# Kernel optimization log

Hardware: AMD Instinct MI355X
Metric: run time of the kernel (lower is better)

## Reference

```python
import jax, jax.numpy as jnp
import numpy as np

B, N, D, H, C = 1, 256, 128, 4, 32
EPS = 1e-5

def setup_inputs() -> dict:
    key = jax.random.key(0)
    ks = jax.random.split(key, 10)
    s = 1.0 / np.sqrt(D)
    return {
        "Z_raw": jax.random.normal(ks[0], (B, N, N, D), dtype=jnp.float32),
        "Z_mask": jnp.ones((B, N, N), dtype=jnp.float32),
        "ln_w": jnp.ones((D,), dtype=jnp.float32),
        "ln_b": jnp.zeros((D,), dtype=jnp.float32),
        "b_proj_w": (jax.random.normal(ks[1], (H, D), dtype=jnp.float32) * s),
        "wq": jax.random.normal(ks[2], (D, H * C), dtype=jnp.float32) * s,
        "wk": jax.random.normal(ks[3], (D, H * C), dtype=jnp.float32) * s,
        "wv": jax.random.normal(ks[4], (D, H * C), dtype=jnp.float32) * s,
        "wg": jax.random.normal(ks[5], (D, H * C), dtype=jnp.float32) * s,
        "bg": jnp.ones((H * C,), dtype=jnp.float32),  # FastFold inits gating bias to 1
        "wo": jax.random.normal(ks[6], (H * C, D), dtype=jnp.float32) / np.sqrt(H * C),
        "out_bias": jnp.zeros((D,), dtype=jnp.float32),
    }

def reference(Z_raw, Z_mask, ln_w, ln_b, b_proj_w, wq, wk, wv, wg, bg, wo, out_bias):
    # LayerNorm over d_pair
    mu = jnp.mean(Z_raw, axis=-1, keepdims=True)
    var = jnp.mean(jnp.square(Z_raw - mu), axis=-1, keepdims=True)
    Z = (Z_raw - mu) * jax.lax.rsqrt(var + EPS) * ln_w + ln_b  # [B,N,N,D]

    # Triangle bias: b[b,h,q,k] (shared across rows i)
    tb = jnp.einsum('bqkd,hd->bhqk', Z, b_proj_w)  # [B,H,N,N]

    scale = 1.0 / np.sqrt(C)
    q = jnp.einsum('bijd,de->bije', Z, wq).reshape(B, N, N, H, C) * scale
    k = jnp.einsum('bijd,de->bije', Z, wk).reshape(B, N, N, H, C)
    v = jnp.einsum('bijd,de->bije', Z, wv).reshape(B, N, N, H, C)

    logits = jnp.einsum('biqhc,bikhc->bihqk', q, k)  # [B,I,H,N,N]
    mask_bias = 1e9 * (Z_mask - 1.0)  # [B,I,J]
    logits = logits + mask_bias[:, :, None, None, :] + tb[:, None]
    attn = jax.nn.softmax(logits, axis=-1)

    o = jnp.einsum('bihqk,bikhc->biqhc', attn, v)  # [B,I,N,H,C]
    gate = jax.nn.sigmoid(jnp.einsum('bijd,de->bije', Z, wg) + bg)
    o = o.reshape(B, N, N, H * C) * gate
    out = jnp.einsum('bije,ed->bijd', o, wo)

    # bias_dropout_add (eval mode: dropout is identity; dropout_mask is ones)
    return Z_raw + out + out_bias
```

## Files before the change

### kernel.cpp

```cpp
#include <hip/hip_runtime.h>
#include <hip/hip_bf16.h>


#define NN 256
#define DD 128
#define NP (NN*NN)

typedef __hip_bfloat16 bf16;
typedef unsigned short u16;
typedef unsigned int u32;
typedef __bf16 bf16x8 __attribute__((ext_vector_type(8)));
typedef short s16x4 __attribute__((ext_vector_type(4)));
typedef float f32x4 __attribute__((ext_vector_type(4)));

__device__ __forceinline__ float b2f(bf16 x) { return __bfloat162float(x); }
__device__ __forceinline__ bf16 f2b(float x) { return __float2bfloat16(x); }
__device__ __forceinline__ float lo16(u32 u) { return __uint_as_float(u << 16); }
__device__ __forceinline__ float hi16(u32 u) { return __uint_as_float(u & 0xFFFF0000u); }
__device__ __forceinline__ float fexp2(float x) { return __builtin_amdgcn_exp2f(x); }
__device__ __forceinline__ bool bf16_mode(const void* lnw_raw) {
    return ((const u32*)lnw_raw)[0] == 0x3F803F80u;
}
__device__ __forceinline__ u32 pk2(float a, float b) {
    union { bf16 h; u16 u; } ca, cb; ca.h = f2b(a); cb.h = f2b(b);
    return ((u32)cb.u << 16) | (u32)ca.u;
}
__device__ __forceinline__ bf16x8 ld_frag(const u32* p) {
    uint4 r = *(const uint4*)p;
    return __builtin_bit_cast(bf16x8, r);
}
#define MFMA16(a,b,c) __builtin_amdgcn_mfma_f32_16x16x32_bf16(a,b,c,0,0,0)
#define MFMA16K(a,b,c) __builtin_amdgcn_mfma_f32_16x16x16bf16_1k(a,b,c,0,0,0)
#define PLANE(et) (((size_t)(et)) << 19)

#define OFF_ZM    0
#define OFF_LNW   65536
#define OFF_LNB   65664
#define OFF_BPW   65792
#define OFF_WQ    66304
#define OFF_WK    82688
#define OFF_WV    99072
#define OFF_WG    115456
#define OFF_BG    131840
#define OFF_WO    131968
#define OFF_OBIAS 148352
#define CANON_TOTAL 148480
#define OFF_WQT   148480
#define OFF_WKT   164864
#define OFF_WVT   181248
#define OFF_WGT   197632
#define OFF_WOT   214016
#define CANONT_TOTAL 81920

#define SCALE 0.17677669529663687f
#define LOG2E 1.4426950408889634f

__global__ __launch_bounds__(256) void k_conv(
    const void* zm, const void* lnw, const void* lnb, const void* bpw,
    const void* wq, const void* wk, const void* wv, const void* wg,
    const void* bg, const void* wo, const void* obias, bf16* canon)
{
    const bool bfm = bf16_mode(lnw);
    int idx = blockIdx.x * 256 + threadIdx.x;
    if (idx < CANON_TOTAL) {
        const void* src; int off;
        if      (idx < OFF_LNW)   { src = zm;    off = idx; }
        else if (idx < OFF_LNB)   { src = lnw;   off = idx - OFF_LNW; }
        else if (idx < OFF_BPW)   { src = lnb;   off = idx - OFF_LNB; }
        else if (idx < OFF_WQ)    { src = bpw;   off = idx - OFF_BPW; }
        else if (idx < OFF_WK)    { src = wq;    off = idx - OFF_WQ; }
        else if (idx < OFF_WV)    { src = wk;    off = idx - OFF_WK; }
        else if (idx < OFF_WG)    { src = wv;    off = idx - OFF_WV; }
        else if (idx < OFF_BG)    { src = wg;    off = idx - OFF_WG; }
        else if (idx < OFF_WO)    { src = bg;    off = idx - OFF_BG; }
        else if (idx < OFF_OBIAS) { src = wo;    off = idx - OFF_WO; }
        else                      { src = obias; off = idx - OFF_OBIAS; }
        float f = bfm ? b2f(((const bf16*)src)[off]) : ((const float*)src)[off];
        if (idx >= OFF_BPW && idx < OFF_WQ) f *= LOG2E;
        if (idx >= OFF_BG  && idx < OFF_WO) f *= LOG2E;
        canon[idx] = f2b(f);
    } else if (idx < CANON_TOTAL + CANONT_TOTAL) {
        int i2 = idx - CANON_TOTAL;
        int m = i2 >> 14, r = i2 & 16383;
        int a = r >> 7, b = r & 127;
        const void* s = (m==0) ? wq : (m==1) ? wk : (m==2) ? wv
                      : (m==3) ? wg : wo;
        float v = bfm ? b2f(((const bf16*)s)[b*128 + a])
                      : ((const float*)s)[b*128 + a];
        if (m == 0) v *= SCALE*LOG2E;
        if (m == 3) v *= LOG2E;
        canon[OFF_WQT + i2] = f2b(v);
    }
}

__global__ __launch_bounds__(256, 4) void k_ln_qkv(
    const void* __restrict__ Zr, const void* __restrict__ lnw_raw,
    const bf16* __restrict__ canon,
    u32* __restrict__ qbw, u32* __restrict__ kbw,
    u32* __restrict__ vbTw, u32* __restrict__ gbw, bf16* __restrict__ tbw)
{
    __shared__ u32 zs[64*68];
    const bool bfm = bf16_mode(lnw_raw);
    const u32* cw = (const u32*)canon;
    const int t = threadIdx.x;
    const int base = blockIdx.x * 64;
    const int p = t >> 2, l = t & 3;
    const int pair = base + p;

    float vals[32];
    if (bfm) {
        const u32* zr = (const u32*)Zr + (size_t)pair*64 + l*16;
        #pragma unroll
        for (int j = 0; j < 16; ++j) {
            u32 u = zr[j];
            vals[2*j] = lo16(u); vals[2*j+1] = hi16(u);
        }
    } else {
        const float* zr = (const float*)Zr + (size_t)pair*128 + l*32;
        #pragma unroll
        for (int j = 0; j < 32; ++j) vals[j] = zr[j];
    }

    float s = 0.f;
    #pragma unroll
    for (int m = 0; m < 32; ++m) s += vals[m];
    s += __shfl_xor(s, 1); s += __shfl_xor(s, 2);
    const float mu = s * (1.f/128.f);
    float s2 = 0.f;
    #pragma unroll
    for (int m = 0; m < 32; ++m) { float d = vals[m] - mu; s2 += d*d; }
    s2 += __shfl_xor(s2, 1); s2 += __shfl_xor(s2, 2);
    const float rstd = rsqrtf(s2 * (1.f/128.f) + 1e-5f);

    const u32* lnw_w = cw + (OFF_LNW>>1) + l*16;
    const u32* lnb_w = cw + (OFF_LNB>>1) + l*16;
    #pragma unroll
    for (int j = 0; j < 16; ++j) {
        u32 uw = lnw_w[j], ub = lnb_w[j];
        float z0 = (vals[2*j]  -mu)*rstd*lo16(uw) + lo16(ub);
        float z1 = (vals[2*j+1]-mu)*rstd*hi16(uw) + hi16(ub);
        zs[p*68 + l*16 + j] = pk2(z0, z1);
    }
    __syncthreads();

    const int wv_ = t >> 6, lane = t & 63, qn = lane & 15, quad = lane >> 4;

    {
        f32x4 dtb = {0.f,0.f,0.f,0.f};
        #pragma unroll
        for (int ks = 0; ks < 4; ++ks) {
            bf16x8 a = ld_frag(cw + (OFF_BPW>>1) + qn*64 + ks*16 + quad*4);
            bf16x8 zbq = ld_frag(&zs[(wv_*16+qn)*68 + ks*16 + quad*4]);
            dtb = MFMA16(a, zbq, dtb);
        }
        if (quad == 0) {
            const int pc = base + wv_*16 + qn;
            tbw[0*NP + pc] = f2b(dtb[0]);
            tbw[1*NP + pc] = f2b(dtb[1]);
            tbw[2*NP + pc] = f2b(dtb[2]);
            tbw[3*NP + pc] = f2b(dtb[3]);
        }
    }

    const int ib = base >> 8;
    const int jbase = (base & 255);

    #pragma unroll
    for (int ei = 0; ei < 2; ++ei) {
        const int et = wv_*2 + ei;
        bf16x8 aq[4], ak[4], av[4], ag[4];
        #pragma unroll
        for (int ks = 0; ks < 4; ++ks) {
            aq[ks] = ld_frag(cw + (OFF_WQT>>1) + (et*16+qn)*64 + ks*16 + quad*4);
            ak[ks] = ld_frag(cw + (OFF_WKT>>1) + (et*16+qn)*64 + ks*16 + quad*4);
            av[ks] = ld_frag(cw + (OFF_WVT>>1) + (et*16+qn)*64 + ks*16 + quad*4);
            ag[ks] = ld_frag(cw + (OFF_WGT>>1) + (et*16+qn)*64 + ks*16 + quad*4);
        }
        const uint2 bgv = *(const uint2*)(cw + (OFF_BG>>1) + et*8 + quad*2);
        const int e = et*16 + qn;
        u32* vrow = vbTw + (size_t)((ib*4 + (e>>5))*32 + (e&31))*128;
        #pragma unroll
        for (int pg = 0; pg < 4; ++pg) {
            bf16x8 zb[4];
            #pragma unroll
            for (int ks = 0; ks < 4; ++ks)
                zb[ks] = ld_frag(&zs[(pg*16+qn)*68 + ks*16 + quad*4]);
            f32x4 dq = {0.f,0.f,0.f,0.f}, dk = {0.f,0.f,0.f,0.f};
            f32x4 dv = {0.f,0.f,0.f,0.f}, dg = {0.f,0.f,0.f,0.f};
            #pragma unroll
            for (int ks = 0; ks < 4; ++ks) {
                dq = MFMA16(aq[ks], zb[ks], dq);
                dk = MFMA16(ak[ks], zb[ks], dk);
                dv = MFMA16(zb[ks], av[ks], dv);
                dg = MFMA16(ag[ks], zb[ks], dg);
            }
            const size_t pr = (size_t)(base + pg*16 + qn)*8 + quad*2;
            uint2 sq; sq.x = pk2(dq[0], dq[1]); sq.y = pk2(dq[2], dq[3]);
            *(uint2*)(qbw + PLANE(et) + pr) = sq;
            uint2 sk; sk.x = pk2(dk[0], dk[1]); sk.y = pk2(dk[2], dk[3]);
            *(uint2*)(kbw + PLANE(et) + pr) = sk;
            float g0 = 1.f / (1.f + fexp2(-(dg[0] + lo16(bgv.x))));
            float g1 = 1.f / (1.f + fexp2(-(dg[1] + hi16(bgv.x))));
            float g2 = 1.f / (1.f + fexp2(-(dg[2] + lo16(bgv.y))));
            float g3 = 1.f / (1.f + fexp2(-(dg[3] + hi16(bgv.y))));
            uint2 sg; sg.x = pk2(g0, g1); sg.y = pk2(g2, g3);
            *(uint2*)(gbw + PLANE(et) + pr) = sg;
            const int jj = jbase + pg*16 + quad*4;
            uint2 sv2; sv2.x = pk2(dv[0], dv[1]); sv2.y = pk2(dv[2], dv[3]);
            *(uint2*)(vrow + (jj>>1)) = sv2;
        }
    }
}

__global__ __launch_bounds__(256, 4) void k_attn(
    const u32* __restrict__ qb, u32* __restrict__ kb,
    const u32* __restrict__ vbT, const bf16* __restrict__ canon,
    const bf16* __restrict__ tbw, const u32* __restrict__ gb)
{
    __shared__ u32 ks_s[256*16];
    __shared__ u32 vs_s[32*128];
    __shared__ float mb_s[256];
    const int t = threadIdx.x;
    const int i = blockIdx.x & 255, h = blockIdx.x >> 8;

    {
        const uint4* kp0 = (const uint4*)(kb + PLANE(2*h)   + (size_t)i*2048);
        const uint4* kp1 = (const uint4*)(kb + PLANE(2*h+1) + (size_t)i*2048);
        #pragma unroll
        for (int r = 0; r < 2; ++r) {
            int q4 = t + 256*r;
            int p = q4 >> 1;
            int c0 = (q4 & 1);
            int c1 = 2 + (q4 & 1);
            uint4 a = kp0[q4];
            *(uint4*)&ks_s[p*16 + ((c0 + (p>>1)) & 3)*4] = a;
            uint4 b = kp1[q4];
            *(uint4*)&ks_s[p*16 + ((c1 + (p>>1)) & 3)*4] = b;
        }
    }
    #pragma unroll
    for (int r = 0; r < 4; ++r) {
        int u = t + 256*r;
        int row = u >> 5, d4 = (u & 31)*4;
        *(uint4*)&vs_s[row*128 + (d4 ^ ((row & 7) << 2))] =
            *(const uint4*)(vbT + (size_t)((i*4+h)*32 + row)*128 + d4);
    }
    {
        u32 w = ((const u32*)canon)[(OFF_ZM>>1) + i*128 + (t>>1)];
        float m = (t & 1) ? hi16(w) : lo16(w);
        mb_s[t] = 1.4426950e9f * (m - 1.f);
    }
    __syncthreads();

    const int wave = t >> 6, lane = t & 63;
    const int qn = lane & 15, quad = lane >> 4;
    const int ksw = ((quad + (qn>>1)) & 3) * 4;
    const int vswz = (qn & 7) << 2;

    const u32* tbbase = (const u32*)tbw + ((size_t)h*NP >> 1) + (wave*64+qn)*128 + quad*2;

    uint2 tA[8], tB[8];
    #pragma unroll
    for (int kk = 0; kk < 8; ++kk) tA[kk] = *(const uint2*)(tbbase + kk*8);

    #pragma unroll
    for (int qt = 0; qt < 4; ++qt) {
        const int qg = wave*64 + qt*16 + qn;
        bf16x8 qf = ld_frag(qb + PLANE(2*h + (quad>>1)) + (size_t)(i*256+qg)*8 + (quad&1)*4);

        float sum = 0.f;
        f32x4 o0a = {0.f,0.f,0.f,0.f}, o0b = {0.f,0.f,0.f,0.f};
        f32x4 o1a = {0.f,0.f,0.f,0.f}, o1b = {0.f,0.f,0.f,0.f};

        {
            f32x4 sv8[8];
            #pragma unroll
            for (int kk = 0; kk < 8; ++kk) {
                f32x4 mb4 = *(const f32x4*)&mb_s[kk*16 + quad*4];
                sv8[kk][0] = lo16(tA[kk].x) + mb4[0];
                sv8[kk][1] = hi16(tA[kk].x) + mb4[1];
                sv8[kk][2] = lo16(tA[kk].y) + mb4[2];
                sv8[kk][3] = hi16(tA[kk].y) + mb4[3];
            }
            #pragma unroll
            for (int kk = 0; kk < 8; ++kk)
                tB[kk] = *(const uint2*)(tbbase + qt*2048 + (8+kk)*8);
            #pragma unroll
            for (int kk = 0; kk < 8; ++kk) {
                bf16x8 kf = ld_frag(&ks_s[(kk*16+qn)*16 + ksw]);
                sv8[kk] = MFMA16(kf, qf, sv8[kk]);
            }
            #pragma unroll
            for (int kk = 0; kk < 8; ++kk) {
                float e0 = fexp2(sv8[kk][0]);
                float e1 = fexp2(sv8[kk][1]);
                float e2 = fexp2(sv8[kk][2]);
                float e3 = fexp2(sv8[kk][3]);
                sum += (e0 + e1) + (e2 + e3);
                uint2 pw2; pw2.x = pk2(e0, e1); pw2.y = pk2(e2, e3);
                s16x4 pf = __builtin_bit_cast(s16x4, pw2);
                const int vcol = (kk*8 + quad*2) ^ vswz;
                s16x4 v0 = __builtin_bit_cast(s16x4, *(const uint2*)&vs_s[qn*128 + vcol]);
                s16x4 v1 = __builtin_bit_cast(s16x4, *(const uint2*)&vs_s[(16+qn)*128 + vcol]);
                if (kk & 1) {
                    o0b = MFMA16K(v0, pf, o0b);
                    o1b = MFMA16K(v1, pf, o1b);
                } else {
                    o0a = MFMA16K(v0, pf, o0a);
                    o1a = MFMA16K(v1, pf, o1a);
                }
            }
            __builtin_amdgcn_sched_barrier(0);
        }
        {
            f32x4 sv8[8];
            #pragma unroll
            for (int kk = 0; kk < 8; ++kk) {
                f32x4 mb4 = *(const f32x4*)&mb_s[(8+kk)*16 + quad*4];
                sv8[kk][0] = lo16(tB[kk].x) + mb4[0];
                sv8[kk][1] = hi16(tB[kk].x) + mb4[1];
                sv8[kk][2] = lo16(tB[kk].y) + mb4[2];
                sv8[kk][3] = hi16(tB[kk].y) + mb4[3];
            }
            if (qt < 3) {
                #pragma unroll
                for (int kk = 0; kk < 8; ++kk)
                    tA[kk] = *(const uint2*)(tbbase + (qt+1)*2048 + kk*8);
            }
            #pragma unroll
            for (int kk = 0; kk < 8; ++kk) {
                const int kt = 8 + kk;
                bf16x8 kf = ld_frag(&ks_s[(kt*16+qn)*16 + ksw]);
                sv8[kk] = MFMA16(kf, qf, sv8[kk]);
            }
            #pragma unroll
            for (int kk = 0; kk < 8; ++kk) {
                const int kt = 8 + kk;
                float e0 = fexp2(sv8[kk][0]);
                float e1 = fexp2(sv8[kk][1]);
                float e2 = fexp2(sv8[kk][2]);
                float e3 = fexp2(sv8[kk][3]);
                sum += (e0 + e1) + (e2 + e3);
                uint2 pw2; pw2.x = pk2(e0, e1); pw2.y = pk2(e2, e3);
                s16x4 pf = __builtin_bit_cast(s16x4, pw2);
                const int vcol = (kt*8 + quad*2) ^ vswz;
                s16x4 v0 = __builtin_bit_cast(s16x4, *(const uint2*)&vs_s[qn*128 + vcol]);
                s16x4 v1 = __builtin_bit_cast(s16x4, *(const uint2*)&vs_s[(16+qn)*128 + vcol]);
                if (kk & 1) {
                    o0b = MFMA16K(v0, pf, o0b);
                    o1b = MFMA16K(v1, pf, o1b);
                } else {
                    o0a = MFMA16K(v0, pf, o0a);
                    o1a = MFMA16K(v1, pf, o1a);
                }
            }
            __builtin_amdgcn_sched_barrier(0);
        }
        sum += __shfl_xor(sum, 16);
        sum += __shfl_xor(sum, 32);
        f32x4 o0 = o0a + o0b;
        f32x4 o1 = o1a + o1b;

        const u32* gpb = gb + PLANE(2*h) + (size_t)(i*256+qg)*8 + quad*2;
        uint2 ga = *(const uint2*)gpb;
        uint2 gc = *(const uint2*)(gpb + (1u<<19));
        const float rinv = 1.f / sum;
        uint2 s0, s1;
        s0.x = pk2(o0[0]*rinv*lo16(ga.x), o0[1]*rinv*hi16(ga.x));
        s0.y = pk2(o0[2]*rinv*lo16(ga.y), o0[3]*rinv*hi16(ga.y));
        s1.x = pk2(o1[0]*rinv*lo16(gc.x), o1[1]*rinv*hi16(gc.x));
        s1.y = pk2(o1[2]*rinv*lo16(gc.y), o1[3]*rinv*hi16(gc.y));
        u32* opb = kb + PLANE(2*h) + (size_t)(i*256+qg)*8 + quad*2;
        *(uint2*)opb = s0;
        *(uint2*)(opb + (1u<<19)) = s1;
    }
}

__global__ __launch_bounds__(256, 4) void k_out(
    const void* __restrict__ Zr, const void* __restrict__ lnw_raw,
    const bf16* __restrict__ canon,
    const u32* __restrict__ obg, void* __restrict__ outp)
{
    const bool bfm = bf16_mode(lnw_raw);
    const u32* cw = (const u32*)canon;
    const int t = threadIdx.x;
    const int base = blockIdx.x * 64;
    const int wv_ = t >> 6, lane = t & 63, qn = lane & 15, quad = lane >> 4;

    bf16x8 awo[2][4];
    uint2 oi2[2];
    #pragma unroll
    for (int di = 0; di < 2; ++di) {
        const int dt = wv_*2 + di;
        #pragma unroll
        for (int ks = 0; ks < 4; ++ks)
            awo[di][ks] = ld_frag(cw + (OFF_WOT>>1) + (dt*16+qn)*64 + ks*16 + quad*4);
        oi2[di] = *(const uint2*)(cw + (OFF_OBIAS>>1) + dt*8 + quad*2);
    }
    #pragma unroll
    for (int pg = 0; pg < 4; ++pg) {
        const size_t pair = base + pg*16 + qn;
        const size_t prow = pair*64;
        bf16x8 ogb[4];
        #pragma unroll
        for (int ks = 0; ks < 4; ++ks)
            ogb[ks] = ld_frag(obg + PLANE(2*ks + (quad>>1)) + pair*8 + (quad&1)*4);
        #pragma unroll
        for (int di = 0; di < 2; ++di) {
            const int dt = wv_*2 + di;
            f32x4 ao = {0.f,0.f,0.f,0.f};
            #pragma unroll
            for (int ks = 0; ks < 4; ++ks) ao = MFMA16(awo[di][ks], ogb[ks], ao);
            const float b0 = lo16(oi2[di].x), b1 = hi16(oi2[di].x);
            const float b2v = lo16(oi2[di].y), b3 = hi16(oi2[di].y);
            if (bfm) {
                uint2 zr2 = *(const uint2*)((const u32*)Zr + prow + dt*8 + quad*2);
                uint2 w;
                w.x = pk2(ao[0] + b0 + lo16(zr2.x), ao[1] + b1 + hi16(zr2.x));
                w.y = pk2(ao[2] + b2v + lo16(zr2.y), ao[3] + b3 + hi16(zr2.y));
                *(uint2*)((u32*)outp + prow + dt*8 + quad*2) = w;
            } else {
                const float* zr = (const float*)Zr + pair*128 + dt*16 + quad*4;
                float4 z4 = *(const float4*)zr;
                float4 w;
                w.x = ao[0] + b0 + z4.x;  w.y = ao[1] + b1 + z4.y;
                w.z = ao[2] + b2v + z4.z; w.w = ao[3] + b3 + z4.w;
                *(float4*)((float*)outp + pair*128 + dt*16 + quad*4) = w;
            }
        }
    }
}

extern "C" void kernel_launch(void* const* d_in, const int* in_sizes, int n_in,
                              void* d_out, int out_size, void* d_ws, size_t ws_size,
                              hipStream_t stream)
{
    const void* Zr    = d_in[0];
    const void* Zm    = d_in[1];
    const void* lnw   = d_in[2];
    const void* lnb   = d_in[3];
    const void* bpw   = d_in[4];
    const void* wq    = d_in[5];
    const void* wk    = d_in[6];
    const void* wv    = d_in[7];
    const void* wg    = d_in[8];
    const void* bg    = d_in[9];
    const void* wo    = d_in[10];
    const void* obias = d_in[11];

    char* ws = (char*)d_ws;
    const size_t M = 16777216;
    u32* gbw   = (u32*)(ws);
    u32* qbw   = (u32*)(ws + 1*M);
    u32* kbw   = (u32*)(ws + 2*M);
    u32* vbTw  = (u32*)(ws + 3*M);
    bf16* tbw  = (bf16*)(ws + 5*M);
    bf16* canon = (bf16*)(ws + 5*M + 1048576);

    hipLaunchKernelGGL(k_conv, dim3((CANON_TOTAL+CANONT_TOTAL+255)/256), dim3(256),
                       0, stream,
                       Zm, lnw, lnb, bpw, wq, wk, wv, wg, bg, wo, obias, canon);
    hipLaunchKernelGGL(k_ln_qkv, dim3(1024), dim3(256), 0, stream,
                       Zr, lnw, canon, qbw, kbw, vbTw, gbw, tbw);
    hipLaunchKernelGGL(k_attn, dim3(1024), dim3(256), 0, stream,
                       qbw, kbw, vbTw, canon, tbw, gbw);
    hipLaunchKernelGGL(k_out, dim3(1024), dim3(256), 0, stream,
                       Zr, lnw, canon, kbw, d_out);
}
```

Baseline: 179.1 us.

## Split attention blocks over query halves and read mask directly from global

The attention grid is doubled so each block handles two of the four query tiles per (row, head), with launch bounds raised to allow more resident blocks. Two blocks now read the same K plane, so the output is written to a separate workspace buffer instead of overwriting K, and the output kernel reads from that buffer. The mask-bias LDS staging is removed; mask values are loaded from global memory and folded in with an fma. The aim is more parallelism and occupancy to hide latency. The cost is that every block still stages the full K and V into LDS, so that traffic doubles.

```diff
diff --git a/kernel.cpp b/kernel.cpp
--- a/kernel.cpp
+++ b/kernel.cpp
@@ -32,6 +32,7 @@
 #define MFMA16(a,b,c) __builtin_amdgcn_mfma_f32_16x16x32_bf16(a,b,c,0,0,0)
 #define MFMA16K(a,b,c) __builtin_amdgcn_mfma_f32_16x16x16bf16_1k(a,b,c,0,0,0)
 #define PLANE(et) (((size_t)(et)) << 19)
+#define BIGC 1.4426950e9f
 
 #define OFF_ZM    0
 #define OFF_LNW   65536
@@ -212,16 +213,17 @@
     }
 }
 
-__global__ __launch_bounds__(256, 4) void k_attn(
-    const u32* __restrict__ qb, u32* __restrict__ kb,
+__global__ __launch_bounds__(256, 5) void k_attn(
+    const u32* __restrict__ qb, const u32* __restrict__ kb,
     const u32* __restrict__ vbT, const bf16* __restrict__ canon,
-    const bf16* __restrict__ tbw, const u32* __restrict__ gb)
+    const bf16* __restrict__ tbw, const u32* __restrict__ gb,
+    u32* __restrict__ ob)
 {
     __shared__ u32 ks_s[256*16];
     __shared__ u32 vs_s[32*128];
-    __shared__ float mb_s[256];
     const int t = threadIdx.x;
-    const int i = blockIdx.x & 255, h = blockIdx.x >> 8;
+    const int i = blockIdx.x & 255, h = (blockIdx.x >> 8) & 3;
+    const int qh = blockIdx.x >> 10;
 
     {
         const uint4* kp0 = (const uint4*)(kb + PLANE(2*h)   + (size_t)i*2048);
@@ -245,11 +247,6 @@
         *(uint4*)&vs_s[row*128 + (d4 ^ ((row & 7) << 2))] =
             *(const uint4*)(vbT + (size_t)((i*4+h)*32 + row)*128 + d4);
     }
-    {
-        u32 w = ((const u32*)canon)[(OFF_ZM>>1) + i*128 + (t>>1)];
-        float m = (t & 1) ? hi16(w) : lo16(w);
-        mb_s[t] = 1.4426950e9f * (m - 1.f);
-    }
     __syncthreads();
 
     const int wave = t >> 6, lane = t & 63;
@@ -257,14 +254,17 @@
     const int ksw = ((quad + (qn>>1)) & 3) * 4;
     const int vswz = (qn & 7) << 2;
 
+    const u32* zmr = (const u32*)canon + (OFF_ZM>>1) + i*128 + quad*2;
     const u32* tbbase = (const u32*)tbw + ((size_t)h*NP >> 1) + (wave*64+qn)*128 + quad*2;
 
     uint2 tA[8], tB[8];
     #pragma unroll
-    for (int kk = 0; kk < 8; ++kk) tA[kk] = *(const uint2*)(tbbase + kk*8);
-
-    #pragma unroll
-    for (int qt = 0; qt < 4; ++qt) {
+    for (int kk = 0; kk < 8; ++kk)
+        tA[kk] = *(const uint2*)(tbbase + qh*2*2048 + kk*8);
+
+    #pragma unroll
+    for (int qi = 0; qi < 2; ++qi) {
+        const int qt = qh*2 + qi;
         const int qg = wave*64 + qt*16 + qn;
         bf16x8 qf = ld_frag(qb + PLANE(2*h + (quad>>1)) + (size_t)(i*256+qg)*8 + (quad&1)*4);
 
@@ -276,11 +276,11 @@
             f32x4 sv8[8];
             #pragma unroll
             for (int kk = 0; kk < 8; ++kk) {
-                f32x4 mb4 = *(const f32x4*)&mb_s[kk*16 + quad*4];
-                sv8[kk][0] = lo16(tA[kk].x) + mb4[0];
-                sv8[kk][1] = hi16(tA[kk].x) + mb4[1];
-                sv8[kk][2] = lo16(tA[kk].y) + mb4[2];
-                sv8[kk][3] = hi16(tA[kk].y) + mb4[3];
+                uint2 zm2 = *(const uint2*)(zmr + kk*8);
+                sv8[kk][0] = fmaf(BIGC, lo16(zm2.x) - 1.f, lo16(tA[kk].x));
+                sv8[kk][1] = fmaf(BIGC, hi16(zm2.x) - 1.f, hi16(tA[kk].x));
+                sv8[kk][2] = fmaf(BIGC, lo16(zm2.y) - 1.f, lo16(tA[kk].y));
+                sv8[kk][3] = fmaf(BIGC, hi16(zm2.y) - 1.f, hi16(tA[kk].y));
             }
             #pragma unroll
             for (int kk = 0; kk < 8; ++kk)
@@ -316,13 +316,14 @@
             f32x4 sv8[8];
             #pragma unroll
             for (int kk = 0; kk < 8; ++kk) {
-                f32x4 mb4 = *(const f32x4*)&mb_s[(8+kk)*16 + quad*4];
-                sv8[kk][0] = lo16(tB[kk].x) + mb4[0];
-                sv8[kk][1] = hi16(tB[kk].x) + mb4[1];
-                sv8[kk][2] = lo16(tB[kk].y) + mb4[2];
-                sv8[kk][3] = hi16(tB[kk].y) + mb4[3];
-            }
-            if (qt < 3) {
+                const int kt = 8 + kk;
+                uint2 zm2 = *(const uint2*)(zmr + kt*8);
+                sv8[kk][0] = fmaf(BIGC, lo16(zm2.x) - 1.f, lo16(tB[kk].x));
+                sv8[kk][1] = fmaf(BIGC, hi16(zm2.x) - 1.f, hi16(tB[kk].x));
+                sv8[kk][2] = fmaf(BIGC, lo16(zm2.y) - 1.f, lo16(tB[kk].y));
+                sv8[kk][3] = fmaf(BIGC, hi16(zm2.y) - 1.f, hi16(tB[kk].y));
+            }
+            if (qi < 1) {
                 #pragma unroll
                 for (int kk = 0; kk < 8; ++kk)
                     tA[kk] = *(const uint2*)(tbbase + (qt+1)*2048 + kk*8);
@@ -370,7 +371,7 @@
         s0.y = pk2(o0[2]*rinv*lo16(ga.y), o0[3]*rinv*hi16(ga.y));
         s1.x = pk2(o1[0]*rinv*lo16(gc.x), o1[1]*rinv*hi16(gc.x));
         s1.y = pk2(o1[2]*rinv*lo16(gc.y), o1[3]*rinv*hi16(gc.y));
-        u32* opb = kb + PLANE(2*h) + (size_t)(i*256+qg)*8 + quad*2;
+        u32* opb = ob + PLANE(2*h) + (size_t)(i*256+qg)*8 + quad*2;
         *(uint2*)opb = s0;
         *(uint2*)(opb + (1u<<19)) = s1;
     }
@@ -454,6 +455,7 @@
     u32* qbw   = (u32*)(ws + 1*M);
     u32* kbw   = (u32*)(ws + 2*M);
     u32* vbTw  = (u32*)(ws + 3*M);
+    u32* obw   = (u32*)(ws + 4*M);
     bf16* tbw  = (bf16*)(ws + 5*M);
     bf16* canon = (bf16*)(ws + 5*M + 1048576);
 
@@ -462,8 +464,8 @@
                        Zm, lnw, lnb, bpw, wq, wk, wv, wg, bg, wo, obias, canon);
     hipLaunchKernelGGL(k_ln_qkv, dim3(1024), dim3(256), 0, stream,
                        Zr, lnw, canon, qbw, kbw, vbTw, gbw, tbw);
-    hipLaunchKernelGGL(k_attn, dim3(1024), dim3(256), 0, stream,
-                       qbw, kbw, vbTw, canon, tbw, gbw);
+    hipLaunchKernelGGL(k_attn, dim3(2048), dim3(256), 0, stream,
+                       qbw, kbw, vbTw, canon, tbw, gbw, obw);
     hipLaunchKernelGGL(k_out, dim3(1024), dim3(256), 0, stream,
-                       Zr, lnw, canon, kbw, d_out);
-}
+                       Zr, lnw, canon, obw, d_out);
+}
```

Measured after the change: 214.0 us. +19.5%, slower.
